# Kernel optimization log

Measured on AMD Instinct MI355X. Metric: run time of the kernel, lower is better.

## Reference

```python
import jax, jax.numpy as jnp
import numpy as np

B, N, H, T = 2048, 512, 20, 3

def setup_inputs() -> dict:
    key = jax.random.key(0)
    ks = jax.random.split(key, 10)
    x = jax.random.normal(ks[0], (B, N, H), dtype=jnp.float32)
    # row-stochastic-ish adjacency so time-step iteration stays numerically tame
    A_in = jax.random.uniform(ks[1], (N, N), dtype=jnp.float32) / N
    std = 0.05
    W3w = jax.random.normal(ks[2], (H, 2 * H), dtype=jnp.float32) * std
    W3u = jax.random.normal(ks[3], (H, H), dtype=jnp.float32) * std
    W4w = jax.random.normal(ks[4], (H, 2 * H), dtype=jnp.float32) * std
    W4u = jax.random.normal(ks[5], (H, H), dtype=jnp.float32) * std
    W5w = jax.random.normal(ks[6], (H, 2 * H), dtype=jnp.float32) * std
    W5u = jax.random.normal(ks[7], (H, H), dtype=jnp.float32) * std
    W_out = jax.random.normal(ks[8], (H, 2 * H), dtype=jnp.float32) * std
    b_out = jnp.zeros((H,), dtype=jnp.float32)
    return {"x": x, "A_in": A_in, "W3w": W3w, "W3u": W3u, "W4w": W4w,
            "W4u": W4u, "W5w": W5w, "W5u": W5u, "W_out": W_out, "b_out": b_out}

def reference(x, A_in, W3w, W3u, W4w, W4u, W5w, W5u, W_out, b_out):
    # x: [B, N, H]; A_in: [N, N]; out-matrix is the transpose of in-matrix.
    A_out = A_in.T
    b, n, h = x.shape
    x_flat = x.reshape(b * n, h)              # original 'input' kept for skip-cat
    nodes = x                                  # batch_aog_nodes [B, N, H]
    outputs = []
    for _ in range(T):
        # aggregation: in- and out-neighborhood bmm, then concat -> [B*N, 2H]
        agg_in = jnp.einsum('nm,bmh->bnh', A_in, nodes)
        agg_out = jnp.einsum('nm,bmh->bnh', A_out, nodes)
        av = jnp.concatenate([agg_in, agg_out], axis=-1).reshape(b * n, 2 * h)
        fn = nodes.reshape(b * n, h)
        # GRU-style gates
        zv = jax.nn.sigmoid(av @ W3w.T + fn @ W3u.T)
        rv = jax.nn.sigmoid(av @ W4w.T + fn @ W4u.T)
        hv = jnp.tanh(av @ W5w.T + (rv * fn) @ W5u.T)
        fn = (1.0 - zv) * fn + zv * hv
        nodes = fn.reshape(b, n, h)
        step = jnp.concatenate([fn, x_flat], axis=1) @ W_out.T + b_out
        outputs.append(step.reshape(b, n, -1))
    return jnp.stack(outputs, axis=0)  # [T, B, N, out]; torch returns this as a list per step
```

## Files before the change

kernel.cpp:

```cpp
#include <hip/hip_runtime.h>
#include <stdint.h>

#define B_SZ 2048
#define N_SZ 512
#define H_SZ 20
#define T_STEPS 3

typedef unsigned short u16;
typedef __attribute__((ext_vector_type(8))) short bf8;
typedef __attribute__((ext_vector_type(4))) float f4;

#define MFMA(a, b, c) __builtin_amdgcn_mfma_f32_16x16x32_bf16((a), (b), (c), 0, 0, 0)

__device__ __forceinline__ u16 f2bf(float f) {
    union { float f; uint32_t u; } v; v.f = f;
    uint32_t u = v.u;
    u += 0x7FFFu + ((u >> 16) & 1u);
    return (u16)(u >> 16);
}
__device__ __forceinline__ float bf2f(u16 h) {
    union { uint32_t u; float f; } v; v.u = ((uint32_t)h) << 16;
    return v.f;
}
__device__ __forceinline__ int scoff(int c, int f) {
    return c * 64 + (((f >> 3) ^ (c & 7)) << 3) + (f & 7);
}
__device__ __forceinline__ float sigm(float x) { return 1.f / (1.f + __expf(-x)); }


__global__ void prep_nodes(const float* __restrict__ x, u16* __restrict__ nodes) {
    __shared__ float xt[N_SZ * H_SZ];
    int b = blockIdx.x;
    const float* xb = x + (size_t)b * N_SZ * H_SZ;
    for (int i = threadIdx.x; i < N_SZ * H_SZ; i += 256) xt[i] = xb[i];
    __syncthreads();
    u16* nb = nodes + (size_t)b * H_SZ * N_SZ;
    for (int i = threadIdx.x; i < H_SZ * N_SZ; i += 256) {
        int h = i / N_SZ, m = i - h * N_SZ;
        nb[i] = f2bf(xt[m * H_SZ + h]);
    }
}

__global__ void prep_xo(const float* __restrict__ x, const float* __restrict__ Wout,
                        const float* __restrict__ bout, u16* __restrict__ xo) {
    int i = blockIdx.x * 256 + threadIdx.x;
    const float* xv = x + (size_t)i * H_SZ;
    float xl[H_SZ];
    #pragma unroll
    for (int h = 0; h < H_SZ; h++) xl[h] = xv[h];
    u16* o = xo + (size_t)i * H_SZ;
    for (int hp = 0; hp < H_SZ; hp++) {
        float s = bout[hp];
        const float* wr = Wout + hp * 2 * H_SZ + H_SZ;
        #pragma unroll
        for (int h = 0; h < H_SZ; h++) s += xl[h] * wr[h];
        o[hp] = f2bf(s);
    }
}

__global__ void prep_afrag(const float* __restrict__ A, u16* __restrict__ pAT,
                           u16* __restrict__ pA) {
    int idx = blockIdx.x * 256 + threadIdx.x;
    int lane = idx & 63;
    int kt = (idx >> 6) & 15;
    int nt = idx >> 10;
    int n = nt * 16 + (lane & 15);
    int k0 = kt * 32 + (lane >> 4) * 8;
    u16* d1 = pAT + (size_t)idx * 8;
    u16* d2 = pA + (size_t)idx * 8;
    #pragma unroll
    for (int j = 0; j < 8; j++) {
        int m = k0 + j;
        d1[j] = f2bf(A[(size_t)n * N_SZ + m]);
        d2[j] = f2bf(A[(size_t)m * N_SZ + n]);
    }
}

__global__ void prep_wfrag(const float* __restrict__ W3w, const float* __restrict__ W3u,
                           const float* __restrict__ W4w, const float* __restrict__ W4u,
                           const float* __restrict__ W5w, const float* __restrict__ W5u,
                           const float* __restrict__ Wout,
                           u16* __restrict__ wbig, u16* __restrict__ whu, u16* __restrict__ wo1) {
    int t = blockIdx.x * 256 + threadIdx.x;
    int lane = t & 63;
    int l16 = lane & 15, quad = lane >> 4;
    if (t < 768) {
        int kt = (t >> 6) & 1;
        int mt = t >> 7;
        int mrow = mt * 16 + l16;
        int g = mrow >> 5, lr = mrow & 31;
        u16* d = wbig + (size_t)t * 8;
        #pragma unroll
        for (int j = 0; j < 8; j++) {
            int k = kt * 32 + quad * 8 + j;
            float v = 0.f;
            if (lr < 20) {
                if (k < 40) {
                    const float* W = (g == 0) ? W3w : (g == 1) ? W4w : W5w;
                    v = W[lr * 40 + k];
                } else if (k < 60 && g < 2) {
                    const float* U = (g == 0) ? W3u : W4u;
                    v = U[lr * 20 + (k - 40)];
                }
            }
            d[j] = f2bf(v);
        }
    } else if (t < 896) {
        int tt = t - 768;
        int mrow = (tt >> 6) * 16 + l16;
        u16* d = whu + (size_t)tt * 8;
        #pragma unroll
        for (int j = 0; j < 8; j++) {
            int k = quad * 8 + j;
            d[j] = f2bf((mrow < 20 && k < 20) ? W5u[mrow * 20 + k] : 0.f);
        }
    } else {
        int tt = t - 896;
        int mrow = (tt >> 6) * 16 + l16;
        u16* d = wo1 + (size_t)tt * 8;
        #pragma unroll
        for (int j = 0; j < 8; j++) {
            int k = quad * 8 + j;
            d[j] = f2bf((mrow < 20 && k < 20) ? Wout[mrow * 40 + k] : 0.f);
        }
    }
}

__global__ void ws_too_small(float* out) { out[0] = 12345.0f; }

__global__ __launch_bounds__(256, 2)
void step_kernel(const u16* __restrict__ pAT, const u16* __restrict__ pA,
                 const u16* __restrict__ wbig, const u16* __restrict__ whu,
                 const u16* __restrict__ wo1, const u16* __restrict__ xo,
                 u16* __restrict__ nodes, float* __restrict__ out, int t_step)
{
    __shared__ __align__(16) u16 lds_all[40 * 512 + 4 * 2048];
    u16* Xs = lds_all;
    int tid = threadIdx.x;
    int wv = tid >> 6, lane = tid & 63;
    int l16 = lane & 15, quad = lane >> 4;
    int b0 = blockIdx.x * 2;
    u16* scw = lds_all + 40 * 512 + wv * 2048;

    const u16* nb = nodes + (size_t)b0 * (H_SZ * N_SZ);
    #pragma unroll
    for (int i = 0; i < 10; i++) {
        int blk = i * 256 + tid;
        int row = blk >> 6, mblk = blk & 63;
        uint4 v = *(const uint4*)(nb + (size_t)row * 512 + mblk * 8);
        *(uint4*)&Xs[row * 512 + ((mblk ^ (row & 7)) << 3)] = v;
    }
    __syncthreads();

    for (int p = 0; p < 4; p++) {
        int nt0 = wv * 8 + p * 2;

        f4 acc[2][3][2];
        #pragma unroll
        for (int a0 = 0; a0 < 2; a0++)
            #pragma unroll
            for (int a1 = 0; a1 < 3; a1++)
                #pragma unroll
                for (int a2 = 0; a2 < 2; a2++)
                    acc[a0][a1][a2] = (f4){0.f, 0.f, 0.f, 0.f};

        for (int kt = 0; kt < 16; kt++) {
            bf8 af[3];
            #pragma unroll
            for (int mt = 0; mt < 3; mt++) {
                int row = mt * 16 + l16;
                int kb = (kt * 4 + quad) ^ (row & 7);
                af[mt] = *(const bf8*)&Xs[row * 512 + kb * 8];
            }
            #pragma unroll
            for (int ntL = 0; ntL < 2; ntL++) {
                size_t fo = ((size_t)((nt0 + ntL) * 16 + kt) * 64 + lane) * 8;
                bf8 bi = *(const bf8*)(pAT + fo);
                bf8 bo = *(const bf8*)(pA + fo);
                #pragma unroll
                for (int mt = 0; mt < 3; mt++) {
                    acc[ntL][mt][0] = MFMA(af[mt], bi, acc[ntL][mt][0]);
                    acc[ntL][mt][1] = MFMA(af[mt], bo, acc[ntL][mt][1]);
                }
            }
        }

        #pragma unroll
        for (int ntL = 0; ntL < 2; ntL++) {
            int nt = nt0 + ntL;
            int nglob = nt * 16 + l16;

            #pragma unroll
            for (int mt = 0; mt < 3; mt++) {
                if (mt < 2 || quad < 2) {
                    int row0 = mt * 16 + quad * 4;
                    int bs = (row0 >= 20) ? 1 : 0;
                    int h0 = row0 - bs * 20;
                    int c = bs * 16 + l16;
                    #pragma unroll
                    for (int r = 0; r < 4; r++) {
                        scw[scoff(c, h0 + r)]      = f2bf(acc[ntL][mt][0][r]);
                        scw[scoff(c, 20 + h0 + r)] = f2bf(acc[ntL][mt][1][r]);
                    }
                }
            }
            {
                int c = lane & 31;
                int h0 = (lane >> 5) * 10;
                int bs = c >> 4, nl = c & 15;
                int m = nt * 16 + nl;
                int mb = m >> 3, mo = m & 7;
                #pragma unroll
                for (int i = 0; i < 10; i++) {
                    int h = h0 + i;
                    int row = bs * 20 + h;
                    u16 v = Xs[row * 512 + ((mb ^ (row & 7)) << 3) + mo];
                    scw[scoff(c, 40 + h)] = v;
                }
                if (lane < 32) {
                    #pragma unroll
                    for (int f = 60; f < 64; f++) scw[scoff(c, f)] = 0;
                }
            }

            f4 g1[6][2];
            #pragma unroll
            for (int a0 = 0; a0 < 6; a0++) { g1[a0][0] = (f4){0,0,0,0}; g1[a0][1] = (f4){0,0,0,0}; }
            #pragma unroll
            for (int kt = 0; kt < 2; kt++) {
                bf8 bfr[2];
                #pragma unroll
                for (int ct = 0; ct < 2; ct++) {
                    int c = ct * 16 + l16;
                    int fb = (kt * 4 + quad) ^ (c & 7);
                    bfr[ct] = *(const bf8*)&scw[c * 64 + fb * 8];
                }
                #pragma unroll
                for (int mt = 0; mt < 6; mt++) {
                    bf8 wf = *(const bf8*)(wbig + ((size_t)(mt * 2 + kt) * 64 + lane) * 8);
                    g1[mt][0] = MFMA(wf, bfr[0], g1[mt][0]);
                    g1[mt][1] = MFMA(wf, bfr[1], g1[mt][1]);
                }
            }

            #pragma unroll
            for (int ct = 0; ct < 2; ct++) {
                int c = ct * 16 + l16;
                #pragma unroll
                for (int r = 0; r < 4; r++) {
                    int hp = quad * 4 + r;
                    float fn = bf2f(scw[scoff(c, 40 + hp)]);
                    scw[scoff(c, hp)] = f2bf(sigm(g1[2][ct][r]) * fn);
                }
                if (quad == 0) {
                    #pragma unroll
                    for (int r = 0; r < 4; r++) {
                        int hp = 16 + r;
                        float fn = bf2f(scw[scoff(c, 40 + hp)]);
                        scw[scoff(c, hp)] = f2bf(sigm(g1[3][ct][r]) * fn);
                    }
                }
            }

            f4 hu[2][2];
            hu[0][0] = (f4){0,0,0,0}; hu[0][1] = (f4){0,0,0,0};
            hu[1][0] = (f4){0,0,0,0}; hu[1][1] = (f4){0,0,0,0};
            #pragma unroll
            for (int ct = 0; ct < 2; ct++) {
                int c = ct * 16 + l16;
                int fb = quad ^ (c & 7);
                bf8 bfr = *(const bf8*)&scw[c * 64 + fb * 8];
                #pragma unroll
                for (int mt = 0; mt < 2; mt++) {
                    bf8 wf = *(const bf8*)(whu + ((size_t)(mt * 64) + lane) * 8);
                    hu[mt][ct] = MFMA(wf, bfr, hu[mt][ct]);
                }
            }

            #pragma unroll
            for (int ct = 0; ct < 2; ct++) {
                int c = ct * 16 + l16;
                size_t nbase = ((size_t)(b0 + ct) * H_SZ) * N_SZ + nglob;
                #pragma unroll
                for (int r = 0; r < 4; r++) {
                    int hp = quad * 4 + r;
                    float fn = bf2f(scw[scoff(c, 40 + hp)]);
                    float z = sigm(g1[0][ct][r]);
                    float hpre = g1[4][ct][r] + hu[0][ct][r];
                    float hv = 2.f / (1.f + __expf(-2.f * hpre)) - 1.f;
                    u16 w = f2bf((1.f - z) * fn + z * hv);
                    nodes[nbase + (size_t)hp * N_SZ] = w;
                    scw[scoff(c, hp)] = w;
                }
                if (quad == 0) {
                    #pragma unroll
                    for (int r = 0; r < 4; r++) {
                        int hp = 16 + r;
                        float fn = bf2f(scw[scoff(c, 40 + hp)]);
                        float z = sigm(g1[1][ct][r]);
                        float hpre = g1[5][ct][r] + hu[1][ct][r];
                        float hv = 2.f / (1.f + __expf(-2.f * hpre)) - 1.f;
                        u16 w = f2bf((1.f - z) * fn + z * hv);
                        nodes[nbase + (size_t)hp * N_SZ] = w;
                        scw[scoff(c, hp)] = w;
                    }
                }
            }

            f4 og[2][2];
            og[0][0] = (f4){0,0,0,0}; og[0][1] = (f4){0,0,0,0};
            og[1][0] = (f4){0,0,0,0}; og[1][1] = (f4){0,0,0,0};
            #pragma unroll
            for (int ct = 0; ct < 2; ct++) {
                int c = ct * 16 + l16;
                int fb = quad ^ (c & 7);
                bf8 bfr = *(const bf8*)&scw[c * 64 + fb * 8];
                #pragma unroll
                for (int mt = 0; mt < 2; mt++) {
                    bf8 wf = *(const bf8*)(wo1 + ((size_t)(mt * 64) + lane) * 8);
                    og[mt][ct] = MFMA(wf, bfr, og[mt][ct]);
                }
            }

            #pragma unroll
            for (int ct = 0; ct < 2; ct++) {
                int bg = b0 + ct;
                size_t xob = ((size_t)bg * N_SZ + nglob) * H_SZ;
                size_t ob = (((size_t)t_step * B_SZ + bg) * N_SZ + nglob) * H_SZ;
                {
                    f4 v;
                    #pragma unroll
                    for (int r = 0; r < 4; r++) v[r] = og[0][ct][r] + bf2f(xo[xob + quad * 4 + r]);
                    *(f4*)(out + ob + quad * 4) = v;
                }
                if (quad == 0) {
                    f4 v;
                    #pragma unroll
                    for (int r = 0; r < 4; r++) v[r] = og[1][ct][r] + bf2f(xo[xob + 16 + r]);
                    *(f4*)(out + ob + 16) = v;
                }
            }
        }
    }
}

#define WS_NODES   0
#define WS_XO      41943040UL
#define WS_PAT     83886080UL
#define WS_PA      84410368UL
#define WS_WBIG    84934656UL
#define WS_WHU     84946944UL
#define WS_WO1     84948992UL
#define WS_NEEDED  84951040UL

extern "C" void kernel_launch(void* const* d_in, const int* in_sizes, int n_in,
                              void* d_out, int out_size, void* d_ws, size_t ws_size,
                              hipStream_t stream) {
    const float* x    = (const float*)d_in[0];
    const float* A    = (const float*)d_in[1];
    const float* W3w  = (const float*)d_in[2];
    const float* W3u  = (const float*)d_in[3];
    const float* W4w  = (const float*)d_in[4];
    const float* W4u  = (const float*)d_in[5];
    const float* W5w  = (const float*)d_in[6];
    const float* W5u  = (const float*)d_in[7];
    const float* Wout = (const float*)d_in[8];
    const float* bout = (const float*)d_in[9];
    float* out = (float*)d_out;

    if (ws_size < WS_NEEDED) {
        ws_too_small<<<1, 1, 0, stream>>>(out);
        return;
    }
    char* ws = (char*)d_ws;
    u16* nodes = (u16*)(ws + WS_NODES);
    u16* xo    = (u16*)(ws + WS_XO);
    u16* pAT   = (u16*)(ws + WS_PAT);
    u16* pA    = (u16*)(ws + WS_PA);
    u16* wbig  = (u16*)(ws + WS_WBIG);
    u16* whu   = (u16*)(ws + WS_WHU);
    u16* wo1   = (u16*)(ws + WS_WO1);

    prep_nodes<<<B_SZ, 256, 0, stream>>>(x, nodes);
    prep_xo<<<(B_SZ * N_SZ) / 256, 256, 0, stream>>>(x, Wout, bout, xo);
    prep_afrag<<<128, 256, 0, stream>>>(A, pAT, pA);
    prep_wfrag<<<4, 256, 0, stream>>>(W3w, W3u, W4w, W4u, W5w, W5u, Wout, wbig, whu, wo1);

    for (int t = 0; t < T_STEPS; t++)
        step_kernel<<<B_SZ / 2, 256, 0, stream>>>(pAT, pA, wbig, whu, wo1, xo, nodes, out, t);
}
```

Before: 875.4 us.

## Process one batch at a time in GRU epilogue, halve scratch LDS, raise occupancy

The gate/epilogue stage now loops over the two batches in the block sequentially, using a 16-column scratch tile per wave instead of 32. This halves per-wave LDS scratch and live accumulator registers, so launch bounds can request three blocks per CU instead of two. LDS writes and the xo reads are also vectorized into packed 64-bit stores and loads. The cost is that each weight fragment is issued with one MFMA per load instead of two, so weight loads are reused less and the MFMA chains are more serialized.

```diff
diff --git a/kernel.cpp b/kernel.cpp
--- a/kernel.cpp
+++ b/kernel.cpp
@@ -21,6 +21,12 @@
 __device__ __forceinline__ float bf2f(u16 h) {
     union { uint32_t u; float f; } v; v.u = ((uint32_t)h) << 16;
     return v.f;
+}
+__device__ __forceinline__ uint32_t pk2(float a, float b) {
+    return (uint32_t)f2bf(a) | ((uint32_t)f2bf(b) << 16);
+}
+__device__ __forceinline__ uint2 pack4(f4 v) {
+    uint2 r; r.x = pk2(v[0], v[1]); r.y = pk2(v[2], v[3]); return r;
 }
 __device__ __forceinline__ int scoff(int c, int f) {
     return c * 64 + (((f >> 3) ^ (c & 7)) << 3) + (f & 7);
@@ -128,19 +134,19 @@
 
 __global__ void ws_too_small(float* out) { out[0] = 12345.0f; }
 
-__global__ __launch_bounds__(256, 2)
+__global__ __launch_bounds__(256, 3)
 void step_kernel(const u16* __restrict__ pAT, const u16* __restrict__ pA,
                  const u16* __restrict__ wbig, const u16* __restrict__ whu,
                  const u16* __restrict__ wo1, const u16* __restrict__ xo,
                  u16* __restrict__ nodes, float* __restrict__ out, int t_step)
 {
-    __shared__ __align__(16) u16 lds_all[40 * 512 + 4 * 2048];
+    __shared__ __align__(16) u16 lds_all[40 * 512 + 4 * 1024];
     u16* Xs = lds_all;
     int tid = threadIdx.x;
     int wv = tid >> 6, lane = tid & 63;
     int l16 = lane & 15, quad = lane >> 4;
     int b0 = blockIdx.x * 2;
-    u16* scw = lds_all + 40 * 512 + wv * 2048;
+    u16* scw = lds_all + 40 * 512 + wv * 1024;
 
     const u16* nb = nodes + (size_t)b0 * (H_SZ * N_SZ);
     #pragma unroll
@@ -191,153 +197,154 @@
             int nglob = nt * 16 + l16;
 
             #pragma unroll
-            for (int mt = 0; mt < 3; mt++) {
-                if (mt < 2 || quad < 2) {
+            for (int bs = 0; bs < 2; bs++) {
+                #pragma unroll
+                for (int mt = 0; mt < 3; mt++) {
                     int row0 = mt * 16 + quad * 4;
-                    int bs = (row0 >= 20) ? 1 : 0;
-                    int h0 = row0 - bs * 20;
-                    int c = bs * 16 + l16;
+                    int bsof = (row0 >= 20) ? 1 : 0;
+                    int h0 = row0 - bsof * 20;
+                    if (row0 < 40 && bsof == bs) {
+                        *(uint2*)&scw[scoff(l16, h0)]      = pack4(acc[ntL][mt][0]);
+                        *(uint2*)&scw[scoff(l16, 20 + h0)] = pack4(acc[ntL][mt][1]);
+                    }
+                }
+                {
+                    int c = l16;
+                    int m = nt * 16 + c;
+                    int mb = m >> 3, mo = m & 7;
+                    int h0f = quad * 5;
+                    #pragma unroll
+                    for (int i = 0; i < 5; i++) {
+                        int h = h0f + i;
+                        int row = bs * 20 + h;
+                        scw[scoff(c, 40 + h)] = Xs[row * 512 + ((mb ^ (row & 7)) << 3) + mo];
+                    }
+                    scw[scoff(c, 60 + quad)] = 0;
+                }
+
+                f4 g1[6];
+                #pragma unroll
+                for (int a0 = 0; a0 < 6; a0++) g1[a0] = (f4){0.f, 0.f, 0.f, 0.f};
+                #pragma unroll
+                for (int kt = 0; kt < 2; kt++) {
+                    int fb = (kt * 4 + quad) ^ (l16 & 7);
+                    bf8 bfr = *(const bf8*)&scw[l16 * 64 + fb * 8];
+                    #pragma unroll
+                    for (int mt = 0; mt < 6; mt++) {
+                        bf8 wf = *(const bf8*)(wbig + ((size_t)(mt * 2 + kt) * 64 + lane) * 8);
+                        g1[mt] = MFMA(wf, bfr, g1[mt]);
+                    }
+                }
+
+                {
+                    int c = l16;
+                    uint2 fl = *(const uint2*)&scw[scoff(c, 40 + quad * 4)];
+                    uint2 rp;
+                    rp.x = pk2(sigm(g1[2][0]) * bf2f((u16)fl.x),
+                               sigm(g1[2][1]) * bf2f((u16)(fl.x >> 16)));
+                    rp.y = pk2(sigm(g1[2][2]) * bf2f((u16)fl.y),
+                               sigm(g1[2][3]) * bf2f((u16)(fl.y >> 16)));
+                    *(uint2*)&scw[scoff(c, quad * 4)] = rp;
+                    if (quad == 0) {
+                        uint2 fl2 = *(const uint2*)&scw[scoff(c, 56)];
+                        uint2 rp2;
+                        rp2.x = pk2(sigm(g1[3][0]) * bf2f((u16)fl2.x),
+                                    sigm(g1[3][1]) * bf2f((u16)(fl2.x >> 16)));
+                        rp2.y = pk2(sigm(g1[3][2]) * bf2f((u16)fl2.y),
+                                    sigm(g1[3][3]) * bf2f((u16)(fl2.y >> 16)));
+                        *(uint2*)&scw[scoff(c, 16)] = rp2;
+                    }
+                }
+
+                f4 hu[2];
+                hu[0] = (f4){0.f, 0.f, 0.f, 0.f};
+                hu[1] = (f4){0.f, 0.f, 0.f, 0.f};
+                {
+                    int fb = quad ^ (l16 & 7);
+                    bf8 bfr = *(const bf8*)&scw[l16 * 64 + fb * 8];
+                    #pragma unroll
+                    for (int mt = 0; mt < 2; mt++) {
+                        bf8 wf = *(const bf8*)(whu + ((size_t)(mt * 64) + lane) * 8);
+                        hu[mt] = MFMA(wf, bfr, hu[mt]);
+                    }
+                }
+
+                {
+                    int c = l16;
+                    size_t nbase = ((size_t)(b0 + bs) * H_SZ) * N_SZ + nglob;
+                    uint2 fl = *(const uint2*)&scw[scoff(c, 40 + quad * 4)];
+                    u16 fnl[4] = {(u16)fl.x, (u16)(fl.x >> 16), (u16)fl.y, (u16)(fl.y >> 16)};
+                    u16 wv4[4];
                     #pragma unroll
                     for (int r = 0; r < 4; r++) {
-                        scw[scoff(c, h0 + r)]      = f2bf(acc[ntL][mt][0][r]);
-                        scw[scoff(c, 20 + h0 + r)] = f2bf(acc[ntL][mt][1][r]);
-                    }
-                }
-            }
-            {
-                int c = lane & 31;
-                int h0 = (lane >> 5) * 10;
-                int bs = c >> 4, nl = c & 15;
-                int m = nt * 16 + nl;
-                int mb = m >> 3, mo = m & 7;
-                #pragma unroll
-                for (int i = 0; i < 10; i++) {
-                    int h = h0 + i;
-                    int row = bs * 20 + h;
-                    u16 v = Xs[row * 512 + ((mb ^ (row & 7)) << 3) + mo];
-                    scw[scoff(c, 40 + h)] = v;
-                }
-                if (lane < 32) {
-                    #pragma unroll
-                    for (int f = 60; f < 64; f++) scw[scoff(c, f)] = 0;
-                }
-            }
-
-            f4 g1[6][2];
-            #pragma unroll
-            for (int a0 = 0; a0 < 6; a0++) { g1[a0][0] = (f4){0,0,0,0}; g1[a0][1] = (f4){0,0,0,0}; }
-            #pragma unroll
-            for (int kt = 0; kt < 2; kt++) {
-                bf8 bfr[2];
-                #pragma unroll
-                for (int ct = 0; ct < 2; ct++) {
-                    int c = ct * 16 + l16;
-                    int fb = (kt * 4 + quad) ^ (c & 7);
-                    bfr[ct] = *(const bf8*)&scw[c * 64 + fb * 8];
-                }
-                #pragma unroll
-                for (int mt = 0; mt < 6; mt++) {
-                    bf8 wf = *(const bf8*)(wbig + ((size_t)(mt * 2 + kt) * 64 + lane) * 8);
-                    g1[mt][0] = MFMA(wf, bfr[0], g1[mt][0]);
-                    g1[mt][1] = MFMA(wf, bfr[1], g1[mt][1]);
-                }
-            }
-
-            #pragma unroll
-            for (int ct = 0; ct < 2; ct++) {
-                int c = ct * 16 + l16;
-                #pragma unroll
-                for (int r = 0; r < 4; r++) {
-                    int hp = quad * 4 + r;
-                    float fn = bf2f(scw[scoff(c, 40 + hp)]);
-                    scw[scoff(c, hp)] = f2bf(sigm(g1[2][ct][r]) * fn);
-                }
-                if (quad == 0) {
-                    #pragma unroll
-                    for (int r = 0; r < 4; r++) {
-                        int hp = 16 + r;
-                        float fn = bf2f(scw[scoff(c, 40 + hp)]);
-                        scw[scoff(c, hp)] = f2bf(sigm(g1[3][ct][r]) * fn);
-                    }
-                }
-            }
-
-            f4 hu[2][2];
-            hu[0][0] = (f4){0,0,0,0}; hu[0][1] = (f4){0,0,0,0};
-            hu[1][0] = (f4){0,0,0,0}; hu[1][1] = (f4){0,0,0,0};
-            #pragma unroll
-            for (int ct = 0; ct < 2; ct++) {
-                int c = ct * 16 + l16;
-                int fb = quad ^ (c & 7);
-                bf8 bfr = *(const bf8*)&scw[c * 64 + fb * 8];
-                #pragma unroll
-                for (int mt = 0; mt < 2; mt++) {
-                    bf8 wf = *(const bf8*)(whu + ((size_t)(mt * 64) + lane) * 8);
-                    hu[mt][ct] = MFMA(wf, bfr, hu[mt][ct]);
-                }
-            }
-
-            #pragma unroll
-            for (int ct = 0; ct < 2; ct++) {
-                int c = ct * 16 + l16;
-                size_t nbase = ((size_t)(b0 + ct) * H_SZ) * N_SZ + nglob;
-                #pragma unroll
-                for (int r = 0; r < 4; r++) {
-                    int hp = quad * 4 + r;
-                    float fn = bf2f(scw[scoff(c, 40 + hp)]);
-                    float z = sigm(g1[0][ct][r]);
-                    float hpre = g1[4][ct][r] + hu[0][ct][r];
-                    float hv = 2.f / (1.f + __expf(-2.f * hpre)) - 1.f;
-                    u16 w = f2bf((1.f - z) * fn + z * hv);
-                    nodes[nbase + (size_t)hp * N_SZ] = w;
-                    scw[scoff(c, hp)] = w;
-                }
-                if (quad == 0) {
-                    #pragma unroll
-                    for (int r = 0; r < 4; r++) {
-                        int hp = 16 + r;
-                        float fn = bf2f(scw[scoff(c, 40 + hp)]);
-                        float z = sigm(g1[1][ct][r]);
-                        float hpre = g1[5][ct][r] + hu[1][ct][r];
+                        int hp = quad * 4 + r;
+                        float fn = bf2f(fnl[r]);
+                        float z = sigm(g1[0][r]);
+                        float hpre = g1[4][r] + hu[0][r];
                         float hv = 2.f / (1.f + __expf(-2.f * hpre)) - 1.f;
                         u16 w = f2bf((1.f - z) * fn + z * hv);
                         nodes[nbase + (size_t)hp * N_SZ] = w;
-                        scw[scoff(c, hp)] = w;
-                    }
-                }
-            }
-
-            f4 og[2][2];
-            og[0][0] = (f4){0,0,0,0}; og[0][1] = (f4){0,0,0,0};
-            og[1][0] = (f4){0,0,0,0}; og[1][1] = (f4){0,0,0,0};
-            #pragma unroll
-            for (int ct = 0; ct < 2; ct++) {
-                int c = ct * 16 + l16;
-                int fb = quad ^ (c & 7);
-                bf8 bfr = *(const bf8*)&scw[c * 64 + fb * 8];
-                #pragma unroll
-                for (int mt = 0; mt < 2; mt++) {
-                    bf8 wf = *(const bf8*)(wo1 + ((size_t)(mt * 64) + lane) * 8);
-                    og[mt][ct] = MFMA(wf, bfr, og[mt][ct]);
-                }
-            }
-
-            #pragma unroll
-            for (int ct = 0; ct < 2; ct++) {
-                int bg = b0 + ct;
-                size_t xob = ((size_t)bg * N_SZ + nglob) * H_SZ;
-                size_t ob = (((size_t)t_step * B_SZ + bg) * N_SZ + nglob) * H_SZ;
-                {
-                    f4 v;
-                    #pragma unroll
-                    for (int r = 0; r < 4; r++) v[r] = og[0][ct][r] + bf2f(xo[xob + quad * 4 + r]);
-                    *(f4*)(out + ob + quad * 4) = v;
-                }
-                if (quad == 0) {
-                    f4 v;
-                    #pragma unroll
-                    for (int r = 0; r < 4; r++) v[r] = og[1][ct][r] + bf2f(xo[xob + 16 + r]);
-                    *(f4*)(out + ob + 16) = v;
+                        wv4[r] = w;
+                    }
+                    uint2 wp;
+                    wp.x = (uint32_t)wv4[0] | ((uint32_t)wv4[1] << 16);
+                    wp.y = (uint32_t)wv4[2] | ((uint32_t)wv4[3] << 16);
+                    *(uint2*)&scw[scoff(c, quad * 4)] = wp;
+                    if (quad == 0) {
+                        uint2 fl2 = *(const uint2*)&scw[scoff(c, 56)];
+                        u16 fnl2[4] = {(u16)fl2.x, (u16)(fl2.x >> 16), (u16)fl2.y, (u16)(fl2.y >> 16)};
+                        u16 wv42[4];
+                        #pragma unroll
+                        for (int r = 0; r < 4; r++) {
+                            int hp = 16 + r;
+                            float fn = bf2f(fnl2[r]);
+                            float z = sigm(g1[1][r]);
+                            float hpre = g1[5][r] + hu[1][r];
+                            float hv = 2.f / (1.f + __expf(-2.f * hpre)) - 1.f;
+                            u16 w = f2bf((1.f - z) * fn + z * hv);
+                            nodes[nbase + (size_t)hp * N_SZ] = w;
+                            wv42[r] = w;
+                        }
+                        uint2 wp2;
+                        wp2.x = (uint32_t)wv42[0] | ((uint32_t)wv42[1] << 16);
+                        wp2.y = (uint32_t)wv42[2] | ((uint32_t)wv42[3] << 16);
+                        *(uint2*)&scw[scoff(c, 16)] = wp2;
+                    }
+                }
+
+                f4 og[2];
+                og[0] = (f4){0.f, 0.f, 0.f, 0.f};
+                og[1] = (f4){0.f, 0.f, 0.f, 0.f};
+                {
+                    int fb = quad ^ (l16 & 7);
+                    bf8 bfr = *(const bf8*)&scw[l16 * 64 + fb * 8];
+                    #pragma unroll
+                    for (int mt = 0; mt < 2; mt++) {
+                        bf8 wf = *(const bf8*)(wo1 + ((size_t)(mt * 64) + lane) * 8);
+                        og[mt] = MFMA(wf, bfr, og[mt]);
+                    }
+                }
+
+                {
+                    int bg = b0 + bs;
+                    size_t xob = ((size_t)bg * N_SZ + nglob) * H_SZ;
+                    size_t ob = (((size_t)t_step * B_SZ + bg) * N_SZ + nglob) * H_SZ;
+                    {
+                        uint2 xp = *(const uint2*)(xo + xob + quad * 4);
+                        u16 xl[4] = {(u16)xp.x, (u16)(xp.x >> 16), (u16)xp.y, (u16)(xp.y >> 16)};
+                        f4 v;
+                        #pragma unroll
+                        for (int r = 0; r < 4; r++) v[r] = og[0][r] + bf2f(xl[r]);
+                        *(f4*)(out + ob + quad * 4) = v;
+                    }
+                    if (quad == 0) {
+                        uint2 xp = *(const uint2*)(xo + xob + 16);
+                        u16 xl[4] = {(u16)xp.x, (u16)(xp.x >> 16), (u16)xp.y, (u16)(xp.y >> 16)};
+                        f4 v;
+                        #pragma unroll
+                        for (int r = 0; r < 4; r++) v[r] = og[1][r] + bf2f(xl[r]);
+                        *(f4*)(out + ob + 16) = v;
+                    }
                 }
             }
         }
```

Result: slower. 1.411 ms (+61.1%).

## Fuse time steps into one kernel and tile the node state layout

Applied to the files above, without the earlier changes.

The three per-step launches become one launch. Each block loops over the time steps for its own pair of batches, reloading node state from global memory after a block barrier. This works because no other block reads those batches. The node buffer moves from [B][H][N] to a tiled [B][N/16][H][16] layout, so per-lane writes of the updated state land in contiguous 16-element runs, and the LDS fill is remapped to match. This removes two launch gaps and tail effects and improves write coalescing, at the cost of more index arithmetic on the load path and a longer-running kernel.

```diff
diff --git a/kernel.cpp b/kernel.cpp
--- a/kernel.cpp
+++ b/kernel.cpp
@@ -34,10 +34,13 @@
     const float* xb = x + (size_t)b * N_SZ * H_SZ;
     for (int i = threadIdx.x; i < N_SZ * H_SZ; i += 256) xt[i] = xb[i];
     __syncthreads();
-    u16* nb = nodes + (size_t)b * H_SZ * N_SZ;
-    for (int i = threadIdx.x; i < H_SZ * N_SZ; i += 256) {
-        int h = i / N_SZ, m = i - h * N_SZ;
-        nb[i] = f2bf(xt[m * H_SZ + h]);
+    u16* nb = nodes + (size_t)b * (N_SZ * H_SZ);
+    for (int i = threadIdx.x; i < N_SZ * H_SZ; i += 256) {
+        int nt = i / 320;
+        int r  = i - nt * 320;
+        int hp = r >> 4, nl = r & 15;
+        int n = nt * 16 + nl;
+        nb[i] = f2bf(xt[n * H_SZ + hp]);
     }
 }
 
@@ -132,7 +135,7 @@
 void step_kernel(const u16* __restrict__ pAT, const u16* __restrict__ pA,
                  const u16* __restrict__ wbig, const u16* __restrict__ whu,
                  const u16* __restrict__ wo1, const u16* __restrict__ xo,
-                 u16* __restrict__ nodes, float* __restrict__ out, int t_step)
+                 u16* __restrict__ nodes, float* __restrict__ out)
 {
     __shared__ __align__(16) u16 lds_all[40 * 512 + 4 * 2048];
     u16* Xs = lds_all;
@@ -142,205 +145,217 @@
     int b0 = blockIdx.x * 2;
     u16* scw = lds_all + 40 * 512 + wv * 2048;
 
-    const u16* nb = nodes + (size_t)b0 * (H_SZ * N_SZ);
-    #pragma unroll
-    for (int i = 0; i < 10; i++) {
-        int blk = i * 256 + tid;
-        int row = blk >> 6, mblk = blk & 63;
-        uint4 v = *(const uint4*)(nb + (size_t)row * 512 + mblk * 8);
-        *(uint4*)&Xs[row * 512 + ((mblk ^ (row & 7)) << 3)] = v;
-    }
-    __syncthreads();
-
-    for (int p = 0; p < 4; p++) {
-        int nt0 = wv * 8 + p * 2;
-
-        f4 acc[2][3][2];
+    const u16* nb = nodes + (size_t)b0 * (N_SZ * H_SZ);
+
+    #pragma unroll 1
+    for (int t = 0; t < T_STEPS; t++) {
         #pragma unroll
-        for (int a0 = 0; a0 < 2; a0++)
+        for (int i = 0; i < 10; i++) {
+            int idx = i * 256 + tid;
+            uint4 v = *(const uint4*)(nb + (size_t)idx * 8);
+            int bs = idx >= 1280 ? 1 : 0;
+            int idxb = idx - bs * 1280;
+            int nt = idxb / 40;
+            int r  = idxb - nt * 40;
+            int hp = r >> 1;
+            int half = r & 1;
+            int row = bs * 20 + hp;
+            int mb = nt * 2 + half;
+            *(uint4*)&Xs[row * 512 + ((mb ^ (row & 7)) << 3)] = v;
+        }
+        __syncthreads();
+
+        for (int p = 0; p < 4; p++) {
+            int nt0 = wv * 8 + p * 2;
+
+            f4 acc[2][3][2];
             #pragma unroll
-            for (int a1 = 0; a1 < 3; a1++)
-                #pragma unroll
-                for (int a2 = 0; a2 < 2; a2++)
-                    acc[a0][a1][a2] = (f4){0.f, 0.f, 0.f, 0.f};
-
-        for (int kt = 0; kt < 16; kt++) {
-            bf8 af[3];
-            #pragma unroll
-            for (int mt = 0; mt < 3; mt++) {
-                int row = mt * 16 + l16;
-                int kb = (kt * 4 + quad) ^ (row & 7);
-                af[mt] = *(const bf8*)&Xs[row * 512 + kb * 8];
+            for (int a0 = 0; a0 < 2; a0++)
+                #pragma unroll
+                for (int a1 = 0; a1 < 3; a1++)
+                    #pragma unroll
+                    for (int a2 = 0; a2 < 2; a2++)
+                        acc[a0][a1][a2] = (f4){0.f, 0.f, 0.f, 0.f};
+
+            for (int kt = 0; kt < 16; kt++) {
+                bf8 af[3];
+                #pragma unroll
+                for (int mt = 0; mt < 3; mt++) {
+                    int row = mt * 16 + l16;
+                    int kb = (kt * 4 + quad) ^ (row & 7);
+                    af[mt] = *(const bf8*)&Xs[row * 512 + kb * 8];
+                }
+                #pragma unroll
+                for (int ntL = 0; ntL < 2; ntL++) {
+                    size_t fo = ((size_t)((nt0 + ntL) * 16 + kt) * 64 + lane) * 8;
+                    bf8 bi = *(const bf8*)(pAT + fo);
+                    bf8 bo = *(const bf8*)(pA + fo);
+                    #pragma unroll
+                    for (int mt = 0; mt < 3; mt++) {
+                        acc[ntL][mt][0] = MFMA(af[mt], bi, acc[ntL][mt][0]);
+                        acc[ntL][mt][1] = MFMA(af[mt], bo, acc[ntL][mt][1]);
+                    }
+                }
             }
+
             #pragma unroll
             for (int ntL = 0; ntL < 2; ntL++) {
-                size_t fo = ((size_t)((nt0 + ntL) * 16 + kt) * 64 + lane) * 8;
-                bf8 bi = *(const bf8*)(pAT + fo);
-                bf8 bo = *(const bf8*)(pA + fo);
+                int nt = nt0 + ntL;
+                int nglob = nt * 16 + l16;
+
                 #pragma unroll
                 for (int mt = 0; mt < 3; mt++) {
-                    acc[ntL][mt][0] = MFMA(af[mt], bi, acc[ntL][mt][0]);
-                    acc[ntL][mt][1] = MFMA(af[mt], bo, acc[ntL][mt][1]);
+                    if (mt < 2 || quad < 2) {
+                        int row0 = mt * 16 + quad * 4;
+                        int bs = (row0 >= 20) ? 1 : 0;
+                        int h0 = row0 - bs * 20;
+                        int c = bs * 16 + l16;
+                        #pragma unroll
+                        for (int r = 0; r < 4; r++) {
+                            scw[scoff(c, h0 + r)]      = f2bf(acc[ntL][mt][0][r]);
+                            scw[scoff(c, 20 + h0 + r)] = f2bf(acc[ntL][mt][1][r]);
+                        }
+                    }
+                }
+                {
+                    int c = lane & 31;
+                    int h0 = (lane >> 5) * 10;
+                    int bs = c >> 4, nl = c & 15;
+                    int m = nt * 16 + nl;
+                    int mb = m >> 3, mo = m & 7;
+                    #pragma unroll
+                    for (int i = 0; i < 10; i++) {
+                        int h = h0 + i;
+                        int row = bs * 20 + h;
+                        u16 v = Xs[row * 512 + ((mb ^ (row & 7)) << 3) + mo];
+                        scw[scoff(c, 40 + h)] = v;
+                    }
+                    if (lane < 32) {
+                        #pragma unroll
+                        for (int f = 60; f < 64; f++) scw[scoff(c, f)] = 0;
+                    }
+                }
+
+                f4 g1[6][2];
+                #pragma unroll
+                for (int a0 = 0; a0 < 6; a0++) { g1[a0][0] = (f4){0,0,0,0}; g1[a0][1] = (f4){0,0,0,0}; }
+                #pragma unroll
+                for (int kt = 0; kt < 2; kt++) {
+                    bf8 bfr[2];
+                    #pragma unroll
+                    for (int ct = 0; ct < 2; ct++) {
+                        int c = ct * 16 + l16;
+                        int fb = (kt * 4 + quad) ^ (c & 7);
+                        bfr[ct] = *(const bf8*)&scw[c * 64 + fb * 8];
+                    }
+                    #pragma unroll
+                    for (int mt = 0; mt < 6; mt++) {
+                        bf8 wf = *(const bf8*)(wbig + ((size_t)(mt * 2 + kt) * 64 + lane) * 8);
+                        g1[mt][0] = MFMA(wf, bfr[0], g1[mt][0]);
+                        g1[mt][1] = MFMA(wf, bfr[1], g1[mt][1]);
+                    }
+                }
+
+                #pragma unroll
+                for (int ct = 0; ct < 2; ct++) {
+                    int c = ct * 16 + l16;
+                    #pragma unroll
+                    for (int r = 0; r < 4; r++) {
+                        int hp = quad * 4 + r;
+                        float fn = bf2f(scw[scoff(c, 40 + hp)]);
+                        scw[scoff(c, hp)] = f2bf(sigm(g1[2][ct][r]) * fn);
+                    }
+                    if (quad == 0) {
+                        #pragma unroll
+                        for (int r = 0; r < 4; r++) {
+                            int hp = 16 + r;
+                            float fn = bf2f(scw[scoff(c, 40 + hp)]);
+                            scw[scoff(c, hp)] = f2bf(sigm(g1[3][ct][r]) * fn);
+                        }
+                    }
+                }
+
+                f4 hu[2][2];
+                hu[0][0] = (f4){0,0,0,0}; hu[0][1] = (f4){0,0,0,0};
+                hu[1][0] = (f4){0,0,0,0}; hu[1][1] = (f4){0,0,0,0};
+                #pragma unroll
+                for (int ct = 0; ct < 2; ct++) {
+                    int c = ct * 16 + l16;
+                    int fb = quad ^ (c & 7);
+                    bf8 bfr = *(const bf8*)&scw[c * 64 + fb * 8];
+                    #pragma unroll
+                    for (int mt = 0; mt < 2; mt++) {
+                        bf8 wf = *(const bf8*)(whu + ((size_t)(mt * 64) + lane) * 8);
+                        hu[mt][ct] = MFMA(wf, bfr, hu[mt][ct]);
+                    }
+                }
+
+                #pragma unroll
+                for (int ct = 0; ct < 2; ct++) {
+                    int c = ct * 16 + l16;
+                    size_t nbase = ((size_t)(b0 + ct) * 32 + nt) * 320 + l16;
+                    #pragma unroll
+                    for (int r = 0; r < 4; r++) {
+                        int hp = quad * 4 + r;
+                        float fn = bf2f(scw[scoff(c, 40 + hp)]);
+                        float z = sigm(g1[0][ct][r]);
+                        float hpre = g1[4][ct][r] + hu[0][ct][r];
+                        float hv = 2.f / (1.f + __expf(-2.f * hpre)) - 1.f;
+                        u16 w = f2bf((1.f - z) * fn + z * hv);
+                        nodes[nbase + (size_t)hp * 16] = w;
+                        scw[scoff(c, hp)] = w;
+                    }
+                    if (quad == 0) {
+                        #pragma unroll
+                        for (int r = 0; r < 4; r++) {
+                            int hp = 16 + r;
+                            float fn = bf2f(scw[scoff(c, 40 + hp)]);
+                            float z = sigm(g1[1][ct][r]);
+                            float hpre = g1[5][ct][r] + hu[1][ct][r];
+                            float hv = 2.f / (1.f + __expf(-2.f * hpre)) - 1.f;
+                            u16 w = f2bf((1.f - z) * fn + z * hv);
+                            nodes[nbase + (size_t)hp * 16] = w;
+                            scw[scoff(c, hp)] = w;
+                        }
+                    }
+                }
+
+                f4 og[2][2];
+                og[0][0] = (f4){0,0,0,0}; og[0][1] = (f4){0,0,0,0};
+                og[1][0] = (f4){0,0,0,0}; og[1][1] = (f4){0,0,0,0};
+                #pragma unroll
+                for (int ct = 0; ct < 2; ct++) {
+                    int c = ct * 16 + l16;
+                    int fb = quad ^ (c & 7);
+                    bf8 bfr = *(const bf8*)&scw[c * 64 + fb * 8];
+                    #pragma unroll
+                    for (int mt = 0; mt < 2; mt++) {
+                        bf8 wf = *(const bf8*)(wo1 + ((size_t)(mt * 64) + lane) * 8);
+                        og[mt][ct] = MFMA(wf, bfr, og[mt][ct]);
+                    }
+                }
+
+                #pragma unroll
+                for (int ct = 0; ct < 2; ct++) {
+                    int bg = b0 + ct;
+                    size_t xob = ((size_t)bg * N_SZ + nglob) * H_SZ;
+                    size_t ob = (((size_t)t * B_SZ + bg) * N_SZ + nglob) * H_SZ;
+                    {
+                        f4 v;
+                        #pragma unroll
+                        for (int r = 0; r < 4; r++) v[r] = og[0][ct][r] + bf2f(xo[xob + quad * 4 + r]);
+                        *(f4*)(out + ob + quad * 4) = v;
+                    }
+                    if (quad == 0) {
+                        f4 v;
+                        #pragma unroll
+                        for (int r = 0; r < 4; r++) v[r] = og[1][ct][r] + bf2f(xo[xob + 16 + r]);
+                        *(f4*)(out + ob + 16) = v;
+                    }
                 }
             }
         }
-
-        #pragma unroll
-        for (int ntL = 0; ntL < 2; ntL++) {
-            int nt = nt0 + ntL;
-            int nglob = nt * 16 + l16;
-
-            #pragma unroll
-            for (int mt = 0; mt < 3; mt++) {
-                if (mt < 2 || quad < 2) {
-                    int row0 = mt * 16 + quad * 4;
-                    int bs = (row0 >= 20) ? 1 : 0;
-                    int h0 = row0 - bs * 20;
-                    int c = bs * 16 + l16;
-                    #pragma unroll
-                    for (int r = 0; r < 4; r++) {
-                        scw[scoff(c, h0 + r)]      = f2bf(acc[ntL][mt][0][r]);
-                        scw[scoff(c, 20 + h0 + r)] = f2bf(acc[ntL][mt][1][r]);
-                    }
-                }
-            }
-            {
-                int c = lane & 31;
-                int h0 = (lane >> 5) * 10;
-                int bs = c >> 4, nl = c & 15;
-                int m = nt * 16 + nl;
-                int mb = m >> 3, mo = m & 7;
-                #pragma unroll
-                for (int i = 0; i < 10; i++) {
-                    int h = h0 + i;
-                    int row = bs * 20 + h;
-                    u16 v = Xs[row * 512 + ((mb ^ (row & 7)) << 3) + mo];
-                    scw[scoff(c, 40 + h)] = v;
-                }
-                if (lane < 32) {
-                    #pragma unroll
-                    for (int f = 60; f < 64; f++) scw[scoff(c, f)] = 0;
-                }
-            }
-
-            f4 g1[6][2];
-            #pragma unroll
-            for (int a0 = 0; a0 < 6; a0++) { g1[a0][0] = (f4){0,0,0,0}; g1[a0][1] = (f4){0,0,0,0}; }
-            #pragma unroll
-            for (int kt = 0; kt < 2; kt++) {
-                bf8 bfr[2];
-                #pragma unroll
-                for (int ct = 0; ct < 2; ct++) {
-                    int c = ct * 16 + l16;
-                    int fb = (kt * 4 + quad) ^ (c & 7);
-                    bfr[ct] = *(const bf8*)&scw[c * 64 + fb * 8];
-                }
-                #pragma unroll
-                for (int mt = 0; mt < 6; mt++) {
-                    bf8 wf = *(const bf8*)(wbig + ((size_t)(mt * 2 + kt) * 64 + lane) * 8);
-                    g1[mt][0] = MFMA(wf, bfr[0], g1[mt][0]);
-                    g1[mt][1] = MFMA(wf, bfr[1], g1[mt][1]);
-                }
-            }
-
-            #pragma unroll
-            for (int ct = 0; ct < 2; ct++) {
-                int c = ct * 16 + l16;
-                #pragma unroll
-                for (int r = 0; r < 4; r++) {
-                    int hp = quad * 4 + r;
-                    float fn = bf2f(scw[scoff(c, 40 + hp)]);
-                    scw[scoff(c, hp)] = f2bf(sigm(g1[2][ct][r]) * fn);
-                }
-                if (quad == 0) {
-                    #pragma unroll
-                    for (int r = 0; r < 4; r++) {
-                        int hp = 16 + r;
-                        float fn = bf2f(scw[scoff(c, 40 + hp)]);
-                        scw[scoff(c, hp)] = f2bf(sigm(g1[3][ct][r]) * fn);
-                    }
-                }
-            }
-
-            f4 hu[2][2];
-            hu[0][0] = (f4){0,0,0,0}; hu[0][1] = (f4){0,0,0,0};
-            hu[1][0] = (f4){0,0,0,0}; hu[1][1] = (f4){0,0,0,0};
-            #pragma unroll
-            for (int ct = 0; ct < 2; ct++) {
-                int c = ct * 16 + l16;
-                int fb = quad ^ (c & 7);
-                bf8 bfr = *(const bf8*)&scw[c * 64 + fb * 8];
-                #pragma unroll
-                for (int mt = 0; mt < 2; mt++) {
-                    bf8 wf = *(const bf8*)(whu + ((size_t)(mt * 64) + lane) * 8);
-                    hu[mt][ct] = MFMA(wf, bfr, hu[mt][ct]);
-                }
-            }
-
-            #pragma unroll
-            for (int ct = 0; ct < 2; ct++) {
-                int c = ct * 16 + l16;
-                size_t nbase = ((size_t)(b0 + ct) * H_SZ) * N_SZ + nglob;
-                #pragma unroll
-                for (int r = 0; r < 4; r++) {
-                    int hp = quad * 4 + r;
-                    float fn = bf2f(scw[scoff(c, 40 + hp)]);
-                    float z = sigm(g1[0][ct][r]);
-                    float hpre = g1[4][ct][r] + hu[0][ct][r];
-                    float hv = 2.f / (1.f + __expf(-2.f * hpre)) - 1.f;
-                    u16 w = f2bf((1.f - z) * fn + z * hv);
-                    nodes[nbase + (size_t)hp * N_SZ] = w;
-                    scw[scoff(c, hp)] = w;
-                }
-                if (quad == 0) {
-                    #pragma unroll
-                    for (int r = 0; r < 4; r++) {
-                        int hp = 16 + r;
-                        float fn = bf2f(scw[scoff(c, 40 + hp)]);
-                        float z = sigm(g1[1][ct][r]);
-                        float hpre = g1[5][ct][r] + hu[1][ct][r];
-                        float hv = 2.f / (1.f + __expf(-2.f * hpre)) - 1.f;
-                        u16 w = f2bf((1.f - z) * fn + z * hv);
-                        nodes[nbase + (size_t)hp * N_SZ] = w;
-                        scw[scoff(c, hp)] = w;
-                    }
-                }
-            }
-
-            f4 og[2][2];
-            og[0][0] = (f4){0,0,0,0}; og[0][1] = (f4){0,0,0,0};
-            og[1][0] = (f4){0,0,0,0}; og[1][1] = (f4){0,0,0,0};
-            #pragma unroll
-            for (int ct = 0; ct < 2; ct++) {
-                int c = ct * 16 + l16;
-                int fb = quad ^ (c & 7);
-                bf8 bfr = *(const bf8*)&scw[c * 64 + fb * 8];
-                #pragma unroll
-                for (int mt = 0; mt < 2; mt++) {
-                    bf8 wf = *(const bf8*)(wo1 + ((size_t)(mt * 64) + lane) * 8);
-                    og[mt][ct] = MFMA(wf, bfr, og[mt][ct]);
-                }
-            }
-
-            #pragma unroll
-            for (int ct = 0; ct < 2; ct++) {
-                int bg = b0 + ct;
-                size_t xob = ((size_t)bg * N_SZ + nglob) * H_SZ;
-                size_t ob = (((size_t)t_step * B_SZ + bg) * N_SZ + nglob) * H_SZ;
-                {
-                    f4 v;
-                    #pragma unroll
-                    for (int r = 0; r < 4; r++) v[r] = og[0][ct][r] + bf2f(xo[xob + quad * 4 + r]);
-                    *(f4*)(out + ob + quad * 4) = v;
-                }
-                if (quad == 0) {
-                    f4 v;
-                    #pragma unroll
-                    for (int r = 0; r < 4; r++) v[r] = og[1][ct][r] + bf2f(xo[xob + 16 + r]);
-                    *(f4*)(out + ob + 16) = v;
-                }
-            }
-        }
+        if (t < T_STEPS - 1) __syncthreads();
     }
 }
 
@@ -386,6 +401,5 @@
     prep_afrag<<<128, 256, 0, stream>>>(A, pAT, pA);
     prep_wfrag<<<4, 256, 0, stream>>>(W3w, W3u, W4w, W4u, W5w, W5u, Wout, wbig, whu, wo1);
 
-    for (int t = 0; t < T_STEPS; t++)
-        step_kernel<<<B_SZ / 2, 256, 0, stream>>>(pAT, pA, wbig, whu, wo1, xo, nodes, out, t);
-}
+    step_kernel<<<B_SZ / 2, 256, 0, stream>>>(pAT, pA, wbig, whu, wo1, xo, nodes, out);
+}
```

Measured after the change: 831.7 us. 1.05x faster.
